# Kernel tuning notes

Measured on AMD Instinct MI355X. Metric: run time of the kernel, lower is better.

Reference implementation:

```python
import jax, jax.numpy as jnp
import numpy as np

N_HEADS = 3
DS_ITERS = 20
EPS = 1e-8
LN_EPS = 1e-5


def rmsnorm(x, w):
    rms = jnp.sqrt(jnp.mean(x * x, axis=-1, keepdims=True) + EPS)
    return x / rms * w


def layernorm(x, w, b):
    m = jnp.mean(x, axis=-1, keepdims=True)
    v = jnp.mean((x - m) ** 2, axis=-1, keepdims=True)
    return (x - m) / jnp.sqrt(v + LN_EPS) * w + b


def sinkhorn(m):
    # m: [b, t, n, n]; global max-shift then exp, 20 alternating row/col normalizations
    m = m - jnp.max(m, axis=(-2, -1), keepdims=True)
    m = jnp.exp(m)
    def body(_, m):
        m = m / (jnp.sum(m, axis=-1, keepdims=True) + EPS)
        m = m / (jnp.sum(m, axis=-2, keepdims=True) + EPS)
        return m
    return jax.lax.fori_loop(0, DS_ITERS, body, m)


def encoder_block(x, ln1_w, ln1_b, Wq, Wk, Wv, Wo, ln2_w, ln2_b, W1, W2):
    # Standard pre-norm ViT encoder block, bias=False, dropout inactive (eval)
    b, t, d = x.shape
    hd = d // N_HEADS
    h = layernorm(x, ln1_w, ln1_b)
    q = (h @ Wq).reshape(b, t, N_HEADS, hd)
    k = (h @ Wk).reshape(b, t, N_HEADS, hd)
    v = (h @ Wv).reshape(b, t, N_HEADS, hd)
    scores = jnp.einsum('bqhd,bkhd->bhqk', q, k) / jnp.sqrt(jnp.asarray(hd, x.dtype))
    attn = jax.nn.softmax(scores, axis=-1)
    o = jnp.einsum('bhqk,bkhd->bqhd', attn, v).reshape(b, t, d) @ Wo
    x = x + o
    h2 = layernorm(x, ln2_w, ln2_b)
    x = x + jax.nn.gelu(h2 @ W1) @ W2
    return x


def setup_inputs() -> dict:
    key = jax.random.key(0)
    ks = jax.random.split(key, 12)
    b, t, n, d = 32, 1024, 4, 192
    nd, mlp = n * d, 768
    std = 0.02
    x = jax.random.normal(ks[0], (b, t, n, d), dtype=jnp.float32)
    b_res = jnp.full((n, n), -10.0, dtype=jnp.float32)
    b_res = b_res.at[jnp.arange(n), jnp.arange(n)].set(0.0)
    return {
        'x': x,
        'norm_w': jnp.ones((nd,), jnp.float32),
        'phi_pre': std * jax.random.normal(ks[1], (nd, n), jnp.float32),
        'phi_post': std * jax.random.normal(ks[2], (nd, n), jnp.float32),
        'phi_res': std * jax.random.normal(ks[3], (nd, n * n), jnp.float32),
        'b_pre': jnp.full((n,), float(np.log(1.0 / (n - 1.0))), jnp.float32),
        'b_post': jnp.zeros((n,), jnp.float32),
        'b_res': b_res,
        'alpha_pre': jnp.asarray(0.001, jnp.float32),
        'alpha_post': jnp.asarray(0.001, jnp.float32),
        'alpha_res': jnp.asarray(0.001, jnp.float32),
        'ln1_w': jnp.ones((d,), jnp.float32),
        'ln1_b': jnp.zeros((d,), jnp.float32),
        'Wq': std * jax.random.normal(ks[4], (d, d), jnp.float32),
        'Wk': std * jax.random.normal(ks[5], (d, d), jnp.float32),
        'Wv': std * jax.random.normal(ks[6], (d, d), jnp.float32),
        'Wo': std * jax.random.normal(ks[7], (d, d), jnp.float32),
        'ln2_w': jnp.ones((d,), jnp.float32),
        'ln2_b': jnp.zeros((d,), jnp.float32),
        'W1': std * jax.random.normal(ks[8], (d, mlp), jnp.float32),
        'W2': std * jax.random.normal(ks[9], (mlp, d), jnp.float32),
    }


def reference(x, norm_w, phi_pre, phi_post, phi_res, b_pre, b_post, b_res,
              alpha_pre, alpha_post, alpha_res,
              ln1_w, ln1_b, Wq, Wk, Wv, Wo, ln2_w, ln2_b, W1, W2):
    b, t, n, d = x.shape
    streams = rmsnorm(x.reshape(b, t, n * d), norm_w)
    pre_tilde = alpha_pre * (streams @ phi_pre) + b_pre              # [b,t,n]
    post_tilde = alpha_post * (streams @ phi_post) + b_post         # [b,t,n]
    res_tilde = alpha_res * (streams @ phi_res) + b_res.reshape(1, 1, n * n)
    h_pre = jax.nn.sigmoid(pre_tilde)
    h_post = 2.0 * jax.nn.sigmoid(post_tilde)
    h_res = sinkhorn(res_tilde.reshape(b, t, n, n))                 # doubly stochastic
    x_res = jnp.einsum('btij,btjd->btid', h_res, x)
    x_in = jnp.einsum('btn,btnd->btd', h_pre, x)
    y = encoder_block(x_in, ln1_w, ln1_b, Wq, Wk, Wv, Wo, ln2_w, ln2_b, W1, W2)
    x_out = y[:, :, None, :] * h_post[..., None]
    return x_res + x_out
```

## Files before the change

### kernel.cpp

```cpp
#include <hip/hip_runtime.h>
#include <hip/hip_bf16.h>
#include <math.h>

#define BATCH 32
#define SEQ   1024
#define NS    4
#define DIM   192
#define ND    768
#define NH    3
#define HD    64
#define MLP   768
#define TOKENS (BATCH*SEQ)

typedef __bf16 bf16;
typedef bf16  bf16x8 __attribute__((ext_vector_type(8)));
typedef bf16  bf16x4 __attribute__((ext_vector_type(4)));
typedef float f32x4  __attribute__((ext_vector_type(4)));

#define MFMA16(a,b,c) __builtin_amdgcn_mfma_f32_16x16x32_bf16(a,b,c,0,0,0)
#define LOG2E 1.44269504088896f

__device__ inline float gelu_tanh(float x) {
    float x3 = x * x * x;
    return 0.5f * x * (1.0f + tanhf(0.7978845608028654f * (x + 0.044715f * x3)));
}

__global__ __launch_bounds__(256) void wprep_kernel(
    const float* __restrict__ Wq, const float* __restrict__ Wk,
    const float* __restrict__ Wv, const float* __restrict__ Wo,
    const float* __restrict__ W1, const float* __restrict__ W2,
    const float* __restrict__ nw, const float* __restrict__ ppre,
    const float* __restrict__ ppost, const float* __restrict__ pres,
    bf16* __restrict__ wqkv, bf16* __restrict__ wot,
    bf16* __restrict__ w1t, bf16* __restrict__ w2t, bf16* __restrict__ phiw)
{
    const int z = blockIdx.z;
    const int x = threadIdx.x, y = threadIdx.y;
    if (z == 6) {
        if (blockIdx.y != 0 || blockIdx.x >= 3) return;
        const int k = blockIdx.x * 256 + y * 32 + x;
        const float w = nw[k];
#pragma unroll
        for (int n = 0; n < 4; n++)  phiw[n * ND + k]     = (bf16)(w * ppre[k*4 + n]);
#pragma unroll
        for (int n = 0; n < 4; n++)  phiw[(4+n) * ND + k] = (bf16)(w * ppost[k*4 + n]);
#pragma unroll
        for (int n = 0; n < 16; n++) phiw[(8+n) * ND + k] = (bf16)(w * pres[k*16 + n]);
#pragma unroll
        for (int n = 24; n < 32; n++) phiw[n * ND + k]    = (bf16)0.f;
        return;
    }
    const float* src; bf16* dst; int K, N; float scale = 1.f;
    switch (z) {
        case 0: src = Wq; dst = wqkv;            K = 192; N = 192;
                scale = 0.125f * LOG2E; break;
        case 1: src = Wk; dst = wqkv + 192*192;  K = 192; N = 192; break;
        case 2: src = Wv; dst = wqkv + 2*192*192;K = 192; N = 192; break;
        case 3: src = Wo; dst = wot;             K = 192; N = 192; break;
        case 4: src = W1; dst = w1t;             K = 192; N = 768; break;
        default:src = W2; dst = w2t;             K = 768; N = 192; break;
    }
    const int n0 = blockIdx.x * 32, k0 = blockIdx.y * 32;
    if (n0 >= N || k0 >= K) return;
    __shared__ float t[32][33];
#pragma unroll
    for (int i = 0; i < 4; i++)
        t[y + 8*i][x] = src[(size_t)(k0 + y + 8*i) * N + n0 + x];
    __syncthreads();
#pragma unroll
    for (int i = 0; i < 4; i++)
        dst[(size_t)(n0 + y + 8*i) * K + k0 + x] = (bf16)(scale * t[x][y + 8*i]);
}

__global__ __launch_bounds__(64) void prep_kernel(
    const float* __restrict__ x, bf16* __restrict__ xb, float* __restrict__ rinv)
{
    const int tok = blockIdx.x, lane = threadIdx.x;
    const float* xt = x + (size_t)tok * ND;
    float4 xv[3];
    float ssq = 0.f;
#pragma unroll
    for (int r = 0; r < 3; r++) {
        xv[r] = ((const float4*)xt)[lane + 64 * r];
        ssq += xv[r].x*xv[r].x + xv[r].y*xv[r].y + xv[r].z*xv[r].z + xv[r].w*xv[r].w;
    }
#pragma unroll
    for (int off = 32; off; off >>= 1) ssq += __shfl_xor(ssq, off);
    if (lane == 0) rinv[tok] = rsqrtf(ssq / (float)ND + 1e-8f);
#pragma unroll
    for (int r = 0; r < 3; r++) {
        bf16x4 o = {(bf16)xv[r].x, (bf16)xv[r].y, (bf16)xv[r].z, (bf16)xv[r].w};
        *(bf16x4*)(xb + (size_t)tok * ND + 4 * (lane + 64 * r)) = o;
    }
}

__global__ __launch_bounds__(256) void dots_kernel(
    const bf16* __restrict__ xb, const bf16* __restrict__ phiw,
    const float* __restrict__ rinv, float* __restrict__ dots)
{
    const int tid = threadIdx.x, lane = tid & 63, w = tid >> 6;
    const int quad = lane >> 4, c = lane & 15;
    const int tok0 = blockIdx.x * 64 + w * 16;

    f32x4 acc0 = {0.f,0.f,0.f,0.f}, acc1 = {0.f,0.f,0.f,0.f};
    const bf16* arow = xb + (size_t)(tok0 + c) * ND + quad * 8;
    const bf16* b0   = phiw + (size_t)c * ND + quad * 8;
    const bf16* b1   = phiw + (size_t)(16 + c) * ND + quad * 8;
#pragma unroll 6
    for (int k0 = 0; k0 < ND; k0 += 32) {
        bf16x8 af  = *(const bf16x8*)(arow + k0);
        bf16x8 bf0 = *(const bf16x8*)(b0 + k0);
        bf16x8 bf1 = *(const bf16x8*)(b1 + k0);
        acc0 = MFMA16(af, bf0, acc0);
        acc1 = MFMA16(af, bf1, acc1);
    }
#pragma unroll
    for (int r = 0; r < 4; r++) {
        const int tok = tok0 + quad * 4 + r;
        const float s = rinv[tok];
        dots[(size_t)tok * 32 + c]      = acc0[r] * s;
        dots[(size_t)tok * 32 + 16 + c] = acc1[r] * s;
    }
}

__global__ __launch_bounds__(256) void sink_kernel(
    const float* __restrict__ dots, const float* __restrict__ b_pre,
    const float* __restrict__ b_post, const float* __restrict__ b_res,
    const float* __restrict__ a_pre, const float* __restrict__ a_post,
    const float* __restrict__ a_res,
    float* __restrict__ hgate, float* __restrict__ hpost)
{
    const int tok = blockIdx.x * 256 + threadIdx.x;
    const float* dt = dots + (size_t)tok * 32;
    float d[24];
#pragma unroll
    for (int i = 0; i < 6; i++) *(float4*)&d[i*4] = *(const float4*)(dt + i*4);

    const float apre = a_pre[0], apost = a_post[0], ares = a_res[0];
    float hpre[4], hpo[4], m[16];
#pragma unroll
    for (int i = 0; i < 4; i++) {
        hpre[i] = 1.f / (1.f + __expf(-(apre  * d[i]     + b_pre[i])));
        hpo[i]  = 2.f / (1.f + __expf(-(apost * d[4 + i] + b_post[i])));
    }
#pragma unroll
    for (int p = 0; p < 16; p++) m[p] = ares * d[8 + p] + b_res[p];

    float gm = m[0];
#pragma unroll
    for (int p = 1; p < 16; p++) gm = fmaxf(gm, m[p]);
#pragma unroll
    for (int p = 0; p < 16; p++) m[p] = __expf(m[p] - gm);

    for (int it = 0; it < 20; it++) {
#pragma unroll
        for (int i = 0; i < 4; i++) {
            const float inv = 1.f / (m[i*4+0] + m[i*4+1] + m[i*4+2] + m[i*4+3] + 1e-8f);
#pragma unroll
            for (int j = 0; j < 4; j++) m[i*4+j] *= inv;
        }
#pragma unroll
        for (int j = 0; j < 4; j++) {
            const float inv = 1.f / (m[0*4+j] + m[1*4+j] + m[2*4+j] + m[3*4+j] + 1e-8f);
#pragma unroll
            for (int i = 0; i < 4; i++) m[i*4+j] *= inv;
        }
    }

    float* hg = hgate + (size_t)tok * 20;
#pragma unroll
    for (int i = 0; i < 4; i++) *(float4*)(hg + i*4) = *(float4*)&m[i*4];
    *(float4*)(hg + 16) = *(float4*)hpre;
    *(float4*)(hpost + (size_t)tok * 4) = *(float4*)hpo;
}

__global__ __launch_bounds__(64) void mix_kernel(
    const bf16* __restrict__ xb, const float* __restrict__ hgate,
    const float* __restrict__ ln1_w, const float* __restrict__ ln1_b,
    float* __restrict__ out, float* __restrict__ xin, bf16* __restrict__ h1)
{
    const int tok = blockIdx.x, lane = threadIdx.x;
    __shared__ float ldsx[ND];

    const bf16* xt = xb + (size_t)tok * ND;
#pragma unroll
    for (int r = 0; r < 3; r++) {
        const bf16x4 v = *(const bf16x4*)(xt + 4 * (lane + 64 * r));
        float4 f = {(float)v[0], (float)v[1], (float)v[2], (float)v[3]};
        ((float4*)ldsx)[lane + 64 * r] = f;
    }

    const float* hg = hgate + (size_t)tok * 20;
    float hres[16], hpre[4];
#pragma unroll
    for (int p = 0; p < 16; p++) hres[p] = hg[p];
#pragma unroll
    for (int i = 0; i < 4; i++) hpre[i] = hg[16 + i];

    __syncthreads();

    float* ot = out + (size_t)tok * ND;
#pragma unroll
    for (int r = 0; r < 3; r++) {
        const int g  = lane + 64 * r;
        const int p0 = 4 * g;
        const int i  = p0 / DIM;
        const int d0 = p0 % DIM;
        float4 o;
        o.x = hres[i*4+0]*ldsx[0*DIM+d0+0] + hres[i*4+1]*ldsx[1*DIM+d0+0]
            + hres[i*4+2]*ldsx[2*DIM+d0+0] + hres[i*4+3]*ldsx[3*DIM+d0+0];
        o.y = hres[i*4+0]*ldsx[0*DIM+d0+1] + hres[i*4+1]*ldsx[1*DIM+d0+1]
            + hres[i*4+2]*ldsx[2*DIM+d0+1] + hres[i*4+3]*ldsx[3*DIM+d0+1];
        o.z = hres[i*4+0]*ldsx[0*DIM+d0+2] + hres[i*4+1]*ldsx[1*DIM+d0+2]
            + hres[i*4+2]*ldsx[2*DIM+d0+2] + hres[i*4+3]*ldsx[3*DIM+d0+2];
        o.w = hres[i*4+0]*ldsx[0*DIM+d0+3] + hres[i*4+1]*ldsx[1*DIM+d0+3]
            + hres[i*4+2]*ldsx[2*DIM+d0+3] + hres[i*4+3]*ldsx[3*DIM+d0+3];
        ((float4*)ot)[g] = o;
    }

    float xi[3];
#pragma unroll
    for (int r = 0; r < 3; r++) {
        const int d = lane + 64 * r;
        xi[r] = hpre[0]*ldsx[d] + hpre[1]*ldsx[DIM+d]
              + hpre[2]*ldsx[2*DIM+d] + hpre[3]*ldsx[3*DIM+d];
    }
    float sum = xi[0] + xi[1] + xi[2];
#pragma unroll
    for (int off = 32; off; off >>= 1) sum += __shfl_xor(sum, off);
    const float mean = sum / (float)DIM;
    float vs = (xi[0]-mean)*(xi[0]-mean) + (xi[1]-mean)*(xi[1]-mean) + (xi[2]-mean)*(xi[2]-mean);
#pragma unroll
    for (int off = 32; off; off >>= 1) vs += __shfl_xor(vs, off);
    const float inv = rsqrtf(vs / (float)DIM + 1e-5f);

    float* xint = xin + (size_t)tok * DIM;
    bf16*  ht   = h1  + (size_t)tok * DIM;
#pragma unroll
    for (int r = 0; r < 3; r++) {
        const int d = lane + 64 * r;
        xint[d] = xi[r];
        ht[d]   = (bf16)((xi[r] - mean) * inv * ln1_w[d] + ln1_b[d]);
    }
}

template<int EPI, int K>
__global__ __launch_bounds__(256) void gemm_bf(
    const bf16* __restrict__ A, const bf16* __restrict__ Bt,
    bf16* __restrict__ Cb, int N)
{
    const int tid = threadIdx.x, lane = tid & 63, w = tid >> 6;
    const int quad = lane >> 4, c = lane & 15;
    const int tok0 = blockIdx.y * 256 + w * 64;
    const int n0   = blockIdx.x * 64;

    f32x4 acc[4][4];
#pragma unroll
    for (int i = 0; i < 4; i++)
#pragma unroll
        for (int j = 0; j < 4; j++) acc[i][j] = (f32x4){0.f,0.f,0.f,0.f};

    const bf16* abase = A + (size_t)(tok0 + c) * K + quad * 8;
    const bf16* bbase = Bt + (size_t)(n0 + c) * K + quad * 8;
#pragma unroll 2
    for (int k0 = 0; k0 < K; k0 += 32) {
        bf16x8 af[4], bfr[4];
#pragma unroll
        for (int mt = 0; mt < 4; mt++)
            af[mt] = *(const bf16x8*)(abase + (size_t)mt * 16 * K + k0);
#pragma unroll
        for (int nt = 0; nt < 4; nt++)
            bfr[nt] = *(const bf16x8*)(bbase + (size_t)nt * 16 * K + k0);
#pragma unroll
        for (int mt = 0; mt < 4; mt++)
#pragma unroll
            for (int nt = 0; nt < 4; nt++)
                acc[mt][nt] = MFMA16(af[mt], bfr[nt], acc[mt][nt]);
    }

#pragma unroll
    for (int mt = 0; mt < 4; mt++)
#pragma unroll
        for (int r = 0; r < 4; r++) {
            const int row = tok0 + mt*16 + quad*4 + r;
#pragma unroll
            for (int nt = 0; nt < 4; nt++) {
                float v = acc[mt][nt][r];
                if (EPI == 2) v = gelu_tanh(v);
                Cb[(size_t)row * N + n0 + nt*16 + c] = (bf16)v;
            }
        }
}

__global__ __launch_bounds__(256) void gemm_wo_ln(
    const bf16* __restrict__ A, const bf16* __restrict__ Bt,
    const float* __restrict__ xin, const float* __restrict__ lw,
    const float* __restrict__ lb, float* __restrict__ x1, bf16* __restrict__ h2)
{
    const int tid = threadIdx.x, lane = tid & 63, w = tid >> 6;
    const int quad = lane >> 4, c = lane & 15;
    const int tok0 = blockIdx.x * 64 + w * 16;

    f32x4 acc[12];
#pragma unroll
    for (int j = 0; j < 12; j++) acc[j] = (f32x4){0.f,0.f,0.f,0.f};

    const bf16* abase = A + (size_t)(tok0 + c) * 192 + quad * 8;
    const bf16* bbase = Bt + (size_t)c * 192 + quad * 8;
#pragma unroll 2
    for (int k0 = 0; k0 < 192; k0 += 32) {
        bf16x8 af = *(const bf16x8*)(abase + k0);
#pragma unroll
        for (int nt = 0; nt < 12; nt++) {
            bf16x8 bfr = *(const bf16x8*)(bbase + (size_t)nt * 16 * 192 + k0);
            acc[nt] = MFMA16(af, bfr, acc[nt]);
        }
    }

#pragma unroll
    for (int r = 0; r < 4; r++) {
        const int row = tok0 + quad*4 + r;
        float v[12], s = 0.f;
#pragma unroll
        for (int nt = 0; nt < 12; nt++) {
            v[nt] = acc[nt][r] + xin[(size_t)row * 192 + nt*16 + c];
            s += v[nt];
        }
#pragma unroll
        for (int off = 1; off < 16; off <<= 1) s += __shfl_xor(s, off);
        const float mean = s / 192.f;
        float vv = 0.f;
#pragma unroll
        for (int nt = 0; nt < 12; nt++) {
            const float d = v[nt] - mean;
            vv += d * d;
        }
#pragma unroll
        for (int off = 1; off < 16; off <<= 1) vv += __shfl_xor(vv, off);
        const float inv = rsqrtf(vv / 192.f + 1e-5f);
#pragma unroll
        for (int nt = 0; nt < 12; nt++) {
            const int col = nt*16 + c;
            x1[(size_t)row * 192 + col] = v[nt];
            h2[(size_t)row * 192 + col] = (bf16)((v[nt] - mean) * inv * lw[col] + lb[col]);
        }
    }
}

__global__ __launch_bounds__(256) void gemm_w2_final(
    const bf16* __restrict__ A, const bf16* __restrict__ Bt,
    const float* __restrict__ x1, const float* __restrict__ hpost,
    float* __restrict__ out)
{
    const int tid = threadIdx.x, lane = tid & 63, w = tid >> 6;
    const int quad = lane >> 4, c = lane & 15;
    const int tok0 = blockIdx.x * 64 + w * 16;

    f32x4 acc[12];
#pragma unroll
    for (int j = 0; j < 12; j++) acc[j] = (f32x4){0.f,0.f,0.f,0.f};

    const bf16* abase = A + (size_t)(tok0 + c) * 768 + quad * 8;
    const bf16* bbase = Bt + (size_t)c * 768 + quad * 8;
#pragma unroll 2
    for (int k0 = 0; k0 < 768; k0 += 32) {
        bf16x8 af = *(const bf16x8*)(abase + k0);
#pragma unroll
        for (int nt = 0; nt < 12; nt++) {
            bf16x8 bfr = *(const bf16x8*)(bbase + (size_t)nt * 16 * 768 + k0);
            acc[nt] = MFMA16(af, bfr, acc[nt]);
        }
    }

#pragma unroll
    for (int r = 0; r < 4; r++) {
        const int row = tok0 + quad*4 + r;
        const float4 hp = *(const float4*)(hpost + (size_t)row * 4);
        float y[12];
#pragma unroll
        for (int nt = 0; nt < 12; nt++)
            y[nt] = acc[nt][r] + x1[(size_t)row * 192 + nt*16 + c];
        float* orow = out + (size_t)row * ND;
#pragma unroll
        for (int i = 0; i < 4; i++) {
            const float h = (i == 0) ? hp.x : (i == 1) ? hp.y : (i == 2) ? hp.z : hp.w;
#pragma unroll
            for (int nt = 0; nt < 12; nt++) {
                const int col = i * 192 + nt*16 + c;
                orow[col] += y[nt] * h;
            }
        }
    }
}

__global__ __launch_bounds__(256) void vtrans_kernel(
    const bf16* __restrict__ qkv, bf16* __restrict__ vt)
{
    __shared__ bf16 t[64][72];
    const int tid = threadIdx.x;
    const int bh = blockIdx.y, b = bh / NH, h = bh % NH;
    const int s0 = blockIdx.x * 64;

#pragma unroll
    for (int i = 0; i < 2; i++) {
        const int chunk = tid + 256 * i;
        const int srow = chunk >> 3, g = chunk & 7;
        *(uint4*)&t[srow][g * 8] =
            *(const uint4*)(qkv + (size_t)(b * SEQ + s0 + srow) * 576 + 384 + h * 64 + g * 8);
    }
    __syncthreads();
#pragma unroll
    for (int i = 0; i < 2; i++) {
        const int chunk = tid + 256 * i;
        const int d = chunk >> 3, sg = chunk & 7;
        bf16x8 v;
#pragma unroll
        for (int j = 0; j < 8; j++) v[j] = t[sg * 8 + j][d];
        *(bf16x8*)(vt + ((size_t)bh * HD + d) * SEQ + s0 + sg * 8) = v;
    }
}

__global__ __launch_bounds__(64) void attn_mfma(
    const bf16* __restrict__ qkv, const bf16* __restrict__ vt,
    bf16* __restrict__ obuf)
{
    __shared__ bf16 Pw[32 * 64];
    const int lane = threadIdx.x;
    const int quad = lane >> 4, c = lane & 15;
    const int bh = blockIdx.y, b = bh / NH, h = bh % NH;
    const int q0 = blockIdx.x * 32;

    const bf16* kbase = qkv + (size_t)b * SEQ * 576 + 192 + h * 64;
    const bf16* vbase = vt + (size_t)bh * HD * SEQ;

    bf16x8 qf[2][2];
#pragma unroll
    for (int mt = 0; mt < 2; mt++)
#pragma unroll
        for (int ch = 0; ch < 2; ch++)
            qf[mt][ch] = *(const bf16x8*)(qkv + (size_t)(b * SEQ + q0 + mt*16 + c) * 576
                                              + h * 64 + ch * 32 + quad * 8);

    f32x4 of[2][4];
    float lst[2][4];
#pragma unroll
    for (int mt = 0; mt < 2; mt++)
#pragma unroll
        for (int r = 0; r < 4; r++) lst[mt][r] = 0.f;
#pragma unroll
    for (int mt = 0; mt < 2; mt++)
#pragma unroll
        for (int dt = 0; dt < 4; dt++) of[mt][dt] = (f32x4){0.f, 0.f, 0.f, 0.f};

#pragma unroll 1
    for (int kt = 0; kt < SEQ / 64; kt++) {
        f32x4 sf[2][4];
#pragma unroll
        for (int mt = 0; mt < 2; mt++)
#pragma unroll
            for (int nt = 0; nt < 4; nt++) sf[mt][nt] = (f32x4){0.f, 0.f, 0.f, 0.f};
#pragma unroll
        for (int ch = 0; ch < 2; ch++) {
            bf16x8 kf[4];
#pragma unroll
            for (int nt = 0; nt < 4; nt++)
                kf[nt] = *(const bf16x8*)(kbase + (size_t)(kt*64 + nt*16 + c) * 576
                                               + ch * 32 + quad * 8);
#pragma unroll
            for (int mt = 0; mt < 2; mt++)
#pragma unroll
                for (int nt = 0; nt < 4; nt++)
                    sf[mt][nt] = MFMA16(qf[mt][ch], kf[nt], sf[mt][nt]);
        }

#pragma unroll
        for (int mt = 0; mt < 2; mt++)
#pragma unroll
            for (int r = 0; r < 4; r++) {
                float rs = 0.f;
#pragma unroll
                for (int nt = 0; nt < 4; nt++) {
                    const float p = exp2f(sf[mt][nt][r]);
                    sf[mt][nt][r] = p;
                    rs += p;
                }
                lst[mt][r] += rs;
            }

#pragma unroll
        for (int mt = 0; mt < 2; mt++)
#pragma unroll
            for (int nt = 0; nt < 4; nt++)
#pragma unroll
                for (int r = 0; r < 4; r++) {
                    const int row = mt*16 + quad*4 + r;
                    const int col = nt*16 + c;
                    Pw[row*64 + (((col >> 3) ^ (row & 7)) * 8) + (col & 7)] =
                        (bf16)sf[mt][nt][r];
                }

#pragma unroll
        for (int ch = 0; ch < 2; ch++) {
            bf16x8 vf[4], pf[2];
#pragma unroll
            for (int dt = 0; dt < 4; dt++)
                vf[dt] = *(const bf16x8*)(vbase + (size_t)(dt*16 + c) * SEQ
                                               + kt*64 + ch*32 + quad*8);
#pragma unroll
            for (int mt = 0; mt < 2; mt++) {
                const int row = mt*16 + c;
                pf[mt] = *(const bf16x8*)(Pw + row*64 + (((ch*4 + quad) ^ (c & 7)) * 8));
            }
#pragma unroll
            for (int mt = 0; mt < 2; mt++)
#pragma unroll
                for (int dt = 0; dt < 4; dt++)
                    of[mt][dt] = MFMA16(pf[mt], vf[dt], of[mt][dt]);
        }
    }

#pragma unroll
    for (int mt = 0; mt < 2; mt++)
#pragma unroll
        for (int r = 0; r < 4; r++) {
            float s = lst[mt][r];
#pragma unroll
            for (int off = 1; off < 16; off <<= 1) s += __shfl_xor(s, off);
            const float inv = 1.0f / s;
            const size_t tok = (size_t)b * SEQ + q0 + mt*16 + quad*4 + r;
#pragma unroll
            for (int dt = 0; dt < 4; dt++)
                obuf[tok * DIM + h*64 + dt*16 + c] = (bf16)(of[mt][dt][r] * inv);
        }
}

extern "C" void kernel_launch(void* const* d_in, const int* in_sizes, int n_in,
                              void* d_out, int out_size, void* d_ws, size_t ws_size,
                              hipStream_t stream) {
    const float* x         = (const float*)d_in[0];
    const float* norm_w    = (const float*)d_in[1];
    const float* phi_pre   = (const float*)d_in[2];
    const float* phi_post  = (const float*)d_in[3];
    const float* phi_res   = (const float*)d_in[4];
    const float* b_pre     = (const float*)d_in[5];
    const float* b_post    = (const float*)d_in[6];
    const float* b_res     = (const float*)d_in[7];
    const float* alpha_pre = (const float*)d_in[8];
    const float* alpha_post= (const float*)d_in[9];
    const float* alpha_res = (const float*)d_in[10];
    const float* ln1_w     = (const float*)d_in[11];
    const float* ln1_b     = (const float*)d_in[12];
    const float* Wq        = (const float*)d_in[13];
    const float* Wk        = (const float*)d_in[14];
    const float* Wv        = (const float*)d_in[15];
    const float* Wo        = (const float*)d_in[16];
    const float* ln2_w     = (const float*)d_in[17];
    const float* ln2_b     = (const float*)d_in[18];
    const float* W1        = (const float*)d_in[19];
    const float* W2        = (const float*)d_in[20];

    float* out = (float*)d_out;
    float* ws  = (float*)d_ws;

    const size_t TBf = (size_t)TOKENS * DIM;
    float* xin   = ws;
    float* x1    = ws + TBf;
    float* hpost = ws + 2 * TBf;
    float* rinv  = hpost + 131072;
    bf16*  phiw  = (bf16*)(rinv + 32768);
    bf16*  wqkv  = phiw + 32 * ND;
    bf16*  wot   = wqkv + 576 * 192;
    bf16*  w1t   = wot + 192 * 192;
    bf16*  w2t   = w1t + 768 * 192;
    float* regAC = (float*)(w2t + 192 * 768);
    bf16*  xb    = (bf16*)regAC;
    bf16*  qkv   = (bf16*)regAC;
    bf16*  vt    = qkv + (size_t)TOKENS * 576;
    bf16*  gbuf  = (bf16*)regAC;
    float* regBD = regAC + 12582912;
    bf16*  h1    = (bf16*)regBD;
    bf16*  obuf  = h1;
    bf16*  h2    = h1 + TBf;
    float* dotsb = regBD + TBf / 2;
    float* hgate = dotsb + (size_t)TOKENS * 32;

    wprep_kernel<<<dim3(24, 24, 7), dim3(32, 8), 0, stream>>>(
        Wq, Wk, Wv, Wo, W1, W2, norm_w, phi_pre, phi_post, phi_res,
        wqkv, wot, w1t, w2t, phiw);

    prep_kernel<<<TOKENS, 64, 0, stream>>>(x, xb, rinv);
    dots_kernel<<<TOKENS / 64, 256, 0, stream>>>(xb, phiw, rinv, dotsb);
    sink_kernel<<<TOKENS / 256, 256, 0, stream>>>(
        dotsb, b_pre, b_post, b_res, alpha_pre, alpha_post, alpha_res, hgate, hpost);
    mix_kernel<<<TOKENS, 64, 0, stream>>>(xb, hgate, ln1_w, ln1_b, out, xin, h1);

    gemm_bf<0, 192><<<dim3(576/64, TOKENS/256), 256, 0, stream>>>(h1, wqkv, qkv, 576);

    vtrans_kernel<<<dim3(SEQ/64, BATCH*NH), 256, 0, stream>>>(qkv, vt);

    attn_mfma<<<dim3(SEQ/32, BATCH*NH), 64, 0, stream>>>(qkv, vt, obuf);

    gemm_wo_ln<<<TOKENS/64, 256, 0, stream>>>(obuf, wot, xin, ln2_w, ln2_b, x1, h2);

    gemm_bf<2, 192><<<dim3(768/64, TOKENS/256), 256, 0, stream>>>(h2, w1t, gbuf, 768);

    gemm_w2_final<<<TOKENS/64, 256, 0, stream>>>(gbuf, w2t, x1, hpost, out);
}
```

Baseline: 628.4 us.

## Pre-swizzle weights into MFMA fragment layout and fuse residual mix into final GEMM

Weight prep now writes each bf16 weight in a tiled layout that matches the 16x16x32 MFMA B-fragment, so every lane loads a contiguous 16-byte chunk instead of striding across rows. The H_res stream mixing moves out of mix_kernel into gemm_w2_final, which reads the original fp32 x and writes out once. This removes the write-then-read-modify-write of the 25 MB output. The final GEMM is also split across three column blocks to raise parallelism, and hgate moves to a dedicated workspace region. The costs are extra reads of fp32 x and hgate in the epilogue, and the A tile being re-read three times.

Result: faster. 550.5 us (-12.4%).

```diff
diff --git a/kernel.cpp b/kernel.cpp
--- a/kernel.cpp
+++ b/kernel.cpp
@@ -35,41 +35,44 @@
     bf16* __restrict__ w1t, bf16* __restrict__ w2t, bf16* __restrict__ phiw)
 {
     const int z = blockIdx.z;
-    const int x = threadIdx.x, y = threadIdx.y;
+    const int tid = blockIdx.x * 256 + threadIdx.x;
     if (z == 6) {
-        if (blockIdx.y != 0 || blockIdx.x >= 3) return;
-        const int k = blockIdx.x * 256 + y * 32 + x;
-        const float w = nw[k];
-#pragma unroll
-        for (int n = 0; n < 4; n++)  phiw[n * ND + k]     = (bf16)(w * ppre[k*4 + n]);
-#pragma unroll
-        for (int n = 0; n < 4; n++)  phiw[(4+n) * ND + k] = (bf16)(w * ppost[k*4 + n]);
-#pragma unroll
-        for (int n = 0; n < 16; n++) phiw[(8+n) * ND + k] = (bf16)(w * pres[k*16 + n]);
-#pragma unroll
-        for (int n = 24; n < 32; n++) phiw[n * ND + k]    = (bf16)0.f;
+        if (tid >= 32 * 96) return;
+        const int n = tid / 96, k8 = tid % 96;
+        const int kch = k8 >> 2, quad = k8 & 3;
+        const int ntile = n >> 4, nc = n & 15;
+        bf16* d = phiw + ((size_t)(ntile * 24 + kch) * 64 + quad * 16 + nc) * 8;
+#pragma unroll
+        for (int e = 0; e < 8; e++) {
+            const int k = k8 * 8 + e;
+            float v;
+            if      (n < 4)  v = ppre [k * 4  + n];
+            else if (n < 8)  v = ppost[k * 4  + n - 4];
+            else if (n < 24) v = pres [k * 16 + n - 8];
+            else             v = 0.f;
+            d[e] = (bf16)(nw[k] * v);
+        }
         return;
     }
     const float* src; bf16* dst; int K, N; float scale = 1.f;
     switch (z) {
         case 0: src = Wq; dst = wqkv;            K = 192; N = 192;
                 scale = 0.125f * LOG2E; break;
-        case 1: src = Wk; dst = wqkv + 192*192;  K = 192; N = 192; break;
-        case 2: src = Wv; dst = wqkv + 2*192*192;K = 192; N = 192; break;
+        case 1: src = Wk; dst = wqkv + 36864;    K = 192; N = 192; break;
+        case 2: src = Wv; dst = wqkv + 73728;    K = 192; N = 192; break;
         case 3: src = Wo; dst = wot;             K = 192; N = 192; break;
         case 4: src = W1; dst = w1t;             K = 192; N = 768; break;
         default:src = W2; dst = w2t;             K = 768; N = 192; break;
     }
-    const int n0 = blockIdx.x * 32, k0 = blockIdx.y * 32;
-    if (n0 >= N || k0 >= K) return;
-    __shared__ float t[32][33];
-#pragma unroll
-    for (int i = 0; i < 4; i++)
-        t[y + 8*i][x] = src[(size_t)(k0 + y + 8*i) * N + n0 + x];
-    __syncthreads();
-#pragma unroll
-    for (int i = 0; i < 4; i++)
-        dst[(size_t)(n0 + y + 8*i) * K + k0 + x] = (bf16)(scale * t[x][y + 8*i]);
+    const int K8 = K >> 3, KC = K >> 5;
+    if (tid >= N * K8) return;
+    const int n = tid / K8, k8 = tid % K8;
+    const int kch = k8 >> 2, quad = k8 & 3;
+    const int ntile = n >> 4, nc = n & 15;
+    bf16* d = dst + ((size_t)(ntile * KC + kch) * 64 + quad * 16 + nc) * 8;
+#pragma unroll
+    for (int e = 0; e < 8; e++)
+        d[e] = (bf16)(scale * src[(size_t)(k8 * 8 + e) * N + n]);
 }
 
 __global__ __launch_bounds__(64) void prep_kernel(
@@ -104,13 +107,13 @@
 
     f32x4 acc0 = {0.f,0.f,0.f,0.f}, acc1 = {0.f,0.f,0.f,0.f};
     const bf16* arow = xb + (size_t)(tok0 + c) * ND + quad * 8;
-    const bf16* b0   = phiw + (size_t)c * ND + quad * 8;
-    const bf16* b1   = phiw + (size_t)(16 + c) * ND + quad * 8;
+    const bf16* bbase = phiw + lane * 8;
 #pragma unroll 6
     for (int k0 = 0; k0 < ND; k0 += 32) {
+        const int kch = k0 >> 5;
         bf16x8 af  = *(const bf16x8*)(arow + k0);
-        bf16x8 bf0 = *(const bf16x8*)(b0 + k0);
-        bf16x8 bf1 = *(const bf16x8*)(b1 + k0);
+        bf16x8 bf0 = *(const bf16x8*)(bbase + (size_t)kch * 512);
+        bf16x8 bf1 = *(const bf16x8*)(bbase + (size_t)(24 + kch) * 512);
         acc0 = MFMA16(af, bf0, acc0);
         acc1 = MFMA16(af, bf1, acc1);
     }
@@ -177,7 +180,7 @@
 __global__ __launch_bounds__(64) void mix_kernel(
     const bf16* __restrict__ xb, const float* __restrict__ hgate,
     const float* __restrict__ ln1_w, const float* __restrict__ ln1_b,
-    float* __restrict__ out, float* __restrict__ xin, bf16* __restrict__ h1)
+    float* __restrict__ xin, bf16* __restrict__ h1)
 {
     const int tok = blockIdx.x, lane = threadIdx.x;
     __shared__ float ldsx[ND];
@@ -190,33 +193,12 @@
         ((float4*)ldsx)[lane + 64 * r] = f;
     }
 
-    const float* hg = hgate + (size_t)tok * 20;
-    float hres[16], hpre[4];
-#pragma unroll
-    for (int p = 0; p < 16; p++) hres[p] = hg[p];
-#pragma unroll
-    for (int i = 0; i < 4; i++) hpre[i] = hg[16 + i];
+    const float* hg = hgate + (size_t)tok * 20 + 16;
+    float hpre[4];
+#pragma unroll
+    for (int i = 0; i < 4; i++) hpre[i] = hg[i];
 
     __syncthreads();
-
-    float* ot = out + (size_t)tok * ND;
-#pragma unroll
-    for (int r = 0; r < 3; r++) {
-        const int g  = lane + 64 * r;
-        const int p0 = 4 * g;
-        const int i  = p0 / DIM;
-        const int d0 = p0 % DIM;
-        float4 o;
-        o.x = hres[i*4+0]*ldsx[0*DIM+d0+0] + hres[i*4+1]*ldsx[1*DIM+d0+0]
-            + hres[i*4+2]*ldsx[2*DIM+d0+0] + hres[i*4+3]*ldsx[3*DIM+d0+0];
-        o.y = hres[i*4+0]*ldsx[0*DIM+d0+1] + hres[i*4+1]*ldsx[1*DIM+d0+1]
-            + hres[i*4+2]*ldsx[2*DIM+d0+1] + hres[i*4+3]*ldsx[3*DIM+d0+1];
-        o.z = hres[i*4+0]*ldsx[0*DIM+d0+2] + hres[i*4+1]*ldsx[1*DIM+d0+2]
-            + hres[i*4+2]*ldsx[2*DIM+d0+2] + hres[i*4+3]*ldsx[3*DIM+d0+2];
-        o.w = hres[i*4+0]*ldsx[0*DIM+d0+3] + hres[i*4+1]*ldsx[1*DIM+d0+3]
-            + hres[i*4+2]*ldsx[2*DIM+d0+3] + hres[i*4+3]*ldsx[3*DIM+d0+3];
-        ((float4*)ot)[g] = o;
-    }
 
     float xi[3];
 #pragma unroll
@@ -253,6 +235,7 @@
     const int quad = lane >> 4, c = lane & 15;
     const int tok0 = blockIdx.y * 256 + w * 64;
     const int n0   = blockIdx.x * 64;
+    const int KC   = K >> 5;
 
     f32x4 acc[4][4];
 #pragma unroll
@@ -261,16 +244,17 @@
         for (int j = 0; j < 4; j++) acc[i][j] = (f32x4){0.f,0.f,0.f,0.f};
 
     const bf16* abase = A + (size_t)(tok0 + c) * K + quad * 8;
-    const bf16* bbase = Bt + (size_t)(n0 + c) * K + quad * 8;
+    const bf16* bbase = Bt + (size_t)(n0 >> 4) * KC * 512 + lane * 8;
 #pragma unroll 2
     for (int k0 = 0; k0 < K; k0 += 32) {
+        const int kch = k0 >> 5;
         bf16x8 af[4], bfr[4];
 #pragma unroll
         for (int mt = 0; mt < 4; mt++)
             af[mt] = *(const bf16x8*)(abase + (size_t)mt * 16 * K + k0);
 #pragma unroll
         for (int nt = 0; nt < 4; nt++)
-            bfr[nt] = *(const bf16x8*)(bbase + (size_t)nt * 16 * K + k0);
+            bfr[nt] = *(const bf16x8*)(bbase + (size_t)(nt * KC + kch) * 512);
 #pragma unroll
         for (int mt = 0; mt < 4; mt++)
 #pragma unroll
@@ -306,13 +290,14 @@
     for (int j = 0; j < 12; j++) acc[j] = (f32x4){0.f,0.f,0.f,0.f};
 
     const bf16* abase = A + (size_t)(tok0 + c) * 192 + quad * 8;
-    const bf16* bbase = Bt + (size_t)c * 192 + quad * 8;
+    const bf16* bbase = Bt + lane * 8;
 #pragma unroll 2
     for (int k0 = 0; k0 < 192; k0 += 32) {
+        const int kch = k0 >> 5;
         bf16x8 af = *(const bf16x8*)(abase + k0);
 #pragma unroll
         for (int nt = 0; nt < 12; nt++) {
-            bf16x8 bfr = *(const bf16x8*)(bbase + (size_t)nt * 16 * 192 + k0);
+            bf16x8 bfr = *(const bf16x8*)(bbase + (size_t)(nt * 6 + kch) * 512);
             acc[nt] = MFMA16(af, bfr, acc[nt]);
         }
     }
@@ -349,25 +334,28 @@
 
 __global__ __launch_bounds__(256) void gemm_w2_final(
     const bf16* __restrict__ A, const bf16* __restrict__ Bt,
-    const float* __restrict__ x1, const float* __restrict__ hpost,
+    const float* __restrict__ x1, const float* __restrict__ x,
+    const float* __restrict__ hgate, const float* __restrict__ hpost,
     float* __restrict__ out)
 {
     const int tid = threadIdx.x, lane = tid & 63, w = tid >> 6;
     const int quad = lane >> 4, c = lane & 15;
     const int tok0 = blockIdx.x * 64 + w * 16;
-
-    f32x4 acc[12];
-#pragma unroll
-    for (int j = 0; j < 12; j++) acc[j] = (f32x4){0.f,0.f,0.f,0.f};
+    const int s = blockIdx.y;
+
+    f32x4 acc[4];
+#pragma unroll
+    for (int j = 0; j < 4; j++) acc[j] = (f32x4){0.f,0.f,0.f,0.f};
 
     const bf16* abase = A + (size_t)(tok0 + c) * 768 + quad * 8;
-    const bf16* bbase = Bt + (size_t)c * 768 + quad * 8;
-#pragma unroll 2
+    const bf16* bbase = Bt + (size_t)(s * 4) * 24 * 512 + lane * 8;
+#pragma unroll 4
     for (int k0 = 0; k0 < 768; k0 += 32) {
+        const int kch = k0 >> 5;
         bf16x8 af = *(const bf16x8*)(abase + k0);
 #pragma unroll
-        for (int nt = 0; nt < 12; nt++) {
-            bf16x8 bfr = *(const bf16x8*)(bbase + (size_t)nt * 16 * 768 + k0);
+        for (int nt = 0; nt < 4; nt++) {
+            bf16x8 bfr = *(const bf16x8*)(bbase + (size_t)(nt * 24 + kch) * 512);
             acc[nt] = MFMA16(af, bfr, acc[nt]);
         }
     }
@@ -375,19 +363,26 @@
 #pragma unroll
     for (int r = 0; r < 4; r++) {
         const int row = tok0 + quad*4 + r;
+        const float* hg = hgate + (size_t)row * 20;
+        float hres[16];
+#pragma unroll
+        for (int p = 0; p < 16; p++) hres[p] = hg[p];
         const float4 hp = *(const float4*)(hpost + (size_t)row * 4);
-        float y[12];
-#pragma unroll
-        for (int nt = 0; nt < 12; nt++)
-            y[nt] = acc[nt][r] + x1[(size_t)row * 192 + nt*16 + c];
+        const float hpi[4] = {hp.x, hp.y, hp.z, hp.w};
+        const float* xrow = x + (size_t)row * ND;
         float* orow = out + (size_t)row * ND;
 #pragma unroll
-        for (int i = 0; i < 4; i++) {
-            const float h = (i == 0) ? hp.x : (i == 1) ? hp.y : (i == 2) ? hp.z : hp.w;
-#pragma unroll
-            for (int nt = 0; nt < 12; nt++) {
-                const int col = i * 192 + nt*16 + c;
-                orow[col] += y[nt] * h;
+        for (int nt = 0; nt < 4; nt++) {
+            const int col = s*64 + nt*16 + c;
+            const float y = acc[nt][r] + x1[(size_t)row * 192 + col];
+            float xv[4];
+#pragma unroll
+            for (int j = 0; j < 4; j++) xv[j] = xrow[j * 192 + col];
+#pragma unroll
+            for (int i = 0; i < 4; i++) {
+                const float xr = hres[i*4+0]*xv[0] + hres[i*4+1]*xv[1]
+                               + hres[i*4+2]*xv[2] + hres[i*4+3]*xv[3];
+                orow[i * 192 + col] = xr + y * hpi[i];
             }
         }
     }
@@ -567,12 +562,13 @@
     float* x1    = ws + TBf;
     float* hpost = ws + 2 * TBf;
     float* rinv  = hpost + 131072;
-    bf16*  phiw  = (bf16*)(rinv + 32768);
-    bf16*  wqkv  = phiw + 32 * ND;
-    bf16*  wot   = wqkv + 576 * 192;
-    bf16*  w1t   = wot + 192 * 192;
-    bf16*  w2t   = w1t + 768 * 192;
-    float* regAC = (float*)(w2t + 192 * 768);
+    float* hgate = rinv + 32768;
+    bf16*  phiw  = (bf16*)(hgate + (size_t)TOKENS*20);
+    bf16*  wqkv  = phiw + 24576;
+    bf16*  wot   = wqkv + 110592;
+    bf16*  w1t   = wot + 36864;
+    bf16*  w2t   = w1t + 147456;
+    float* regAC = (float*)(w2t + 147456);
     bf16*  xb    = (bf16*)regAC;
     bf16*  qkv   = (bf16*)regAC;
     bf16*  vt    = qkv + (size_t)TOKENS * 576;
@@ -582,9 +578,8 @@
     bf16*  obuf  = h1;
     bf16*  h2    = h1 + TBf;
     float* dotsb = regBD + TBf / 2;
-    float* hgate = dotsb + (size_t)TOKENS * 32;
-
-    wprep_kernel<<<dim3(24, 24, 7), dim3(32, 8), 0, stream>>>(
+
+    wprep_kernel<<<dim3(72, 1, 7), 256, 0, stream>>>(
         Wq, Wk, Wv, Wo, W1, W2, norm_w, phi_pre, phi_post, phi_res,
         wqkv, wot, w1t, w2t, phiw);
 
@@ -592,7 +587,7 @@
     dots_kernel<<<TOKENS / 64, 256, 0, stream>>>(xb, phiw, rinv, dotsb);
     sink_kernel<<<TOKENS / 256, 256, 0, stream>>>(
         dotsb, b_pre, b_post, b_res, alpha_pre, alpha_post, alpha_res, hgate, hpost);
-    mix_kernel<<<TOKENS, 64, 0, stream>>>(xb, hgate, ln1_w, ln1_b, out, xin, h1);
+    mix_kernel<<<TOKENS, 64, 0, stream>>>(xb, hgate, ln1_w, ln1_b, xin, h1);
 
     gemm_bf<0, 192><<<dim3(576/64, TOKENS/256), 256, 0, stream>>>(h1, wqkv, qkv, 576);
 
@@ -604,5 +599,6 @@
 
     gemm_bf<2, 192><<<dim3(768/64, TOKENS/256), 256, 0, stream>>>(h2, w1t, gbuf, 768);
 
-    gemm_w2_final<<<TOKENS/64, 256, 0, stream>>>(gbuf, w2t, x1, hpost, out);
-}
+    gemm_w2_final<<<dim3(TOKENS/64, 3), 256, 0, stream>>>(
+        gbuf, w2t, x1, x, hgate, hpost, out);
+}
```
